# Kernel tuning notes

Measured on AMD Instinct MI355X. Metric: run time of the kernel, lower is better.

Reference implementation:

```python
import jax, jax.numpy as jnp
import numpy as np
import math

B, C, H, W = 16, 256, 96, 96
S = 3  # num_stages
OUT_C = 64


def _pos_encoding(c, h, w):
    # Faithful vectorization of generate_fixed_cosine_positional_encoding.
    pos_y = jnp.linspace(0.0, 1.0, h)
    pos_x = jnp.linspace(0.0, 1.0, w)
    py, px = jnp.meshgrid(pos_y, pos_x, indexing='ij')  # [H, W]
    i_vals = np.arange(0, c // 2, 2)                    # loop indices i
    freqs = jnp.exp(jnp.asarray(i_vals, jnp.float32) * -(math.log(10000.0) / (c // 2)))  # div_term[i//2]
    sin_part = jnp.sin(px[None] * freqs[:, None, None]) + jnp.sin(py[None] * freqs[:, None, None])
    cos_part = jnp.cos(px[None] * freqs[:, None, None]) + jnp.cos(py[None] * freqs[:, None, None])
    pe = jnp.zeros((c, h, w), jnp.float32)
    pe = pe.at[2 * i_vals].set(sin_part).at[2 * i_vals + 1].set(cos_part)
    return pe


def _nearest_resize(wmap, h, w):
    # torch F.interpolate(mode='nearest'): src_idx = floor(dst_idx * in/out)
    hw, ww = wmap.shape[-2], wmap.shape[-1]
    ih = (jnp.arange(h) * hw) // h
    iw = (jnp.arange(w) * ww) // w
    return wmap[..., ih[:, None], iw[None, :]]


def _conv1x1(x, w, b):
    return jnp.einsum('oc,bchw->bohw', w, x) + b[None, :, None, None]


def setup_inputs():
    key = jax.random.key(0)
    ks = jax.random.split(key, 12)
    sc = 0.3 / math.sqrt(C)
    return {
        'x1': jax.random.normal(ks[0], (B, C, H, W), jnp.float32),
        'x2': jax.random.normal(ks[1], (B, C, H, W), jnp.float32),
        'weight_vis': jax.random.uniform(ks[2], (B, H, W), jnp.float32),
        'weight_ir': jax.random.uniform(ks[3], (B, H, W), jnp.float32),
        'q_w': jax.random.normal(ks[4], (S, C, C), jnp.float32) * sc,
        'q_b': jnp.zeros((S, C), jnp.float32),
        'k_w': jax.random.normal(ks[5], (S, C, C), jnp.float32) * sc,
        'k_b': jnp.zeros((S, C), jnp.float32),
        'v_w': jax.random.normal(ks[6], (S, C, C), jnp.float32) * sc,
        'v_b': jnp.zeros((S, C), jnp.float32),
        'proj_w': jax.random.normal(ks[7], (OUT_C, C), jnp.float32) * sc,
        'proj_b': jnp.zeros((OUT_C,), jnp.float32),
    }


def reference(x1, x2, weight_vis, weight_ir, q_w, q_b, k_w, k_b, v_w, v_b, proj_w, proj_b):
    pe = _pos_encoding(x1.shape[1], x1.shape[2], x1.shape[3])  # combined_pos_encoding = pe1
    h, w = x1.shape[2], x1.shape[3]
    w_vis = _nearest_resize(weight_vis[:, None], h, w)  # [B,1,H,W]
    w_ir = _nearest_resize(weight_ir[:, None], h, w)
    fused = x1
    for i in range(S):
        x1 = x1 * w_vis
        x2 = x2 * w_ir
        q = _conv1x1(x1, q_w[i], q_b[i]) + pe[None]          # [B,C,H,W]
        k = _conv1x1(x2, k_w[i], k_b[i]) + pe[None]
        v = _conv1x1(x2, v_w[i], v_b[i])
        logits = jnp.einsum('bchw,bcgw->bchg', q, k)         # per-channel QK^T: [B,C,H,H]
        attn = jax.nn.softmax(logits, axis=-1)
        fused = jnp.einsum('bchg,bcgw->bchw', attn, v)       # [B,C,H,W]
        x1, x2 = fused, fused
    return _conv1x1(fused, proj_w, proj_b)                    # [B,64,H,W]
```

## Files before the change

### kernel.cpp

```cpp
#include <hip/hip_runtime.h>
#include <hip/hip_bf16.h>
#include <math.h>

#define NPOS 9216
#define PERB 2359296ull

typedef unsigned short u16;
typedef __attribute__((ext_vector_type(8))) short short8;
typedef __attribute__((ext_vector_type(4))) float f32x4;

__device__ inline u16 bfhi(float x) {
    unsigned int b = __float_as_uint(x);
    return (u16)((b + 0x7FFFu + ((b >> 16) & 1u)) >> 16);
}
__device__ inline float bf2f(u16 u) { return __uint_as_float(((unsigned int)u) << 16); }

typedef const __attribute__((address_space(1))) void* gvp;
typedef __attribute__((address_space(3))) void* lvp;
__device__ __forceinline__ void glds16(const void* g, void* l) {
    __builtin_amdgcn_global_load_lds((gvp)g, (lvp)l, 16, 0, 0);
}

__global__ __launch_bounds__(256) void tt_kernel(float* __restrict__ T)
{
    int idx = blockIdx.x * 256 + threadIdx.x;
    int c = idx / 96, p = idx - (idx / 96) * 96;
    int j = c >> 2, r = c & 3;
    float f = expf(-(float)(2 * j) * 0.07195578415f);
    float x = (float)p * (1.0f / 95.0f) * f;
    T[idx] = (r == 0) ? sinf(x) : (r == 1) ? cosf(x) : 0.0f;
}

__global__ __launch_bounds__(256) void wsplit(
    const float* __restrict__ qw, const float* __restrict__ kw,
    const float* __restrict__ vw, u16* __restrict__ whi, u16* __restrict__ wlo)
{
    int bid = blockIdx.x;
    int s = bid / 48, rem = bid % 48;
    int mat = rem / 16, rem2 = rem % 16;
    int mb = rem2 / 8, kb = rem2 % 8;
    const float* W = ((mat == 0) ? qw : (mat == 1) ? kw : vw) + (size_t)s * 65536;
    int t = threadIdx.x;
    int m = t >> 1, kh = (t & 1) * 16;
    const float* src = W + (size_t)(mb * 128 + m) * 256 + kb * 32 + kh;
    int s0 = kh >> 3;
    int sw = (m >> 1) & 3;
    size_t ob = (size_t)s * 196608 + (size_t)((mat * 2 + mb) * 8 + kb) * 4096
              + (size_t)m * 32;
    u16 hv[16], lv[16];
#pragma unroll
    for (int j = 0; j < 16; ++j) {
        float x = src[j];
        u16 h = bfhi(x);
        hv[j] = h;
        lv[j] = bfhi(x - bf2f(h));
    }
    *(uint4*)(whi + ob + ((s0 ^ sw) * 8))       = *(uint4*)hv;
    *(uint4*)(whi + ob + (((s0 + 1) ^ sw) * 8)) = *(uint4*)(hv + 8);
    *(uint4*)(wlo + ob + ((s0 ^ sw) * 8))       = *(uint4*)lv;
    *(uint4*)(wlo + ob + (((s0 + 1) ^ sw) * 8)) = *(uint4*)(lv + 8);
}

__global__ __launch_bounds__(512, 4) void gemm_qkv_mfma(
    const u16* __restrict__ whi, const u16* __restrict__ wlo,
    const float* __restrict__ srcq, const float* __restrict__ srckv,
    const float* __restrict__ qb, const float* __restrict__ kbias,
    const float* __restrict__ vb, const float* __restrict__ wvis,
    const float* __restrict__ wir, const float* __restrict__ Ttab,
    float* __restrict__ qo, float* __restrict__ ko, float* __restrict__ vo)
{
    __shared__ char LDSBUF[49152];
    u16* AH = (u16*)LDSBUF;
    u16* AL = AH + 8192;
    u16* BH = AL + 8192;
    u16* BL = BH + 4096;

    int t = threadIdx.x;
    int d = blockIdx.x + 3 * blockIdx.y;
    int role = (d & 7) * 27 + (d >> 3);
    int mat = role / 72, bn = role % 72;
    int b = blockIdx.z;

    const float* gB = ((mat == 0) ? srcq : srckv) + (size_t)b * PERB + bn * 128;
    const u16* gA0 = whi + (size_t)(mat * 2) * 32768;
    const u16* gA1 = wlo + (size_t)(mat * 2) * 32768;

    int wv = t >> 6;
    int wm = wv >> 1, wn = wv & 1;
    int rr = t & 15, gq = (t >> 4) & 3;

    int sxor = (gq ^ ((rr >> 1) & 3)) * 8;
    int offA0 = (wm * 64 + rr) * 32 + sxor;
    int offB0 = (wn * 64 + rr) * 32 + sxor;

    int arow = t >> 2, acol = (t & 3) * 8;
    size_t asrc0 = (size_t)arow * 32 + acol;
    size_t asrc1 = 32768 + (size_t)arow * 32 + acol;

    int bn_ = t & 127, bkh = t >> 7;
    int key = (bn_ >> 1) & 3;
    int wrB = bn_ * 32 + ((bkh ^ key) * 8);
    const float* bp = gB + (size_t)(bkh * 8) * NPOS + bn_;

    f32x4 acc[4][4];
#pragma unroll
    for (int i = 0; i < 4; ++i)
#pragma unroll
        for (int j = 0; j < 4; ++j) acc[i][j] = (f32x4){0.f, 0.f, 0.f, 0.f};

    float xv[8];
#pragma unroll
    for (int j = 0; j < 8; ++j) xv[j] = bp[(size_t)j * NPOS];

    for (int kq = 0; kq < 8; ++kq) {
        {
            glds16(gA0 + kq * 4096 + asrc0, &AH[t * 8]);
            glds16(gA0 + kq * 4096 + asrc1, &AH[t * 8 + 4096]);
            glds16(gA1 + kq * 4096 + asrc0, &AL[t * 8]);
            glds16(gA1 + kq * 4096 + asrc1, &AL[t * 8 + 4096]);
        }
        {
            u16 hv[8], lv[8];
#pragma unroll
            for (int j = 0; j < 8; ++j) {
                float x = xv[j];
                u16 h = bfhi(x);
                hv[j] = h;
                lv[j] = bfhi(x - bf2f(h));
            }
            *(uint4*)(&BH[wrB]) = *(uint4*)hv;
            *(uint4*)(&BL[wrB]) = *(uint4*)lv;
        }
        __syncthreads();

        if (kq < 7) {
#pragma unroll
            for (int j = 0; j < 8; ++j)
                xv[j] = bp[(size_t)((kq + 1) * 32 + j) * NPOS];
        }

        short8 bh[4], bl[4];
#pragma unroll
        for (int r = 0; r < 4; ++r) {
            bh[r] = *(const short8*)(&BH[offB0 + r * 512]);
            bl[r] = *(const short8*)(&BL[offB0 + r * 512]);
        }
#pragma unroll
        for (int f = 0; f < 4; ++f) {
            short8 ah = *(const short8*)(&AH[offA0 + f * 512]);
            short8 al = *(const short8*)(&AL[offA0 + f * 512]);
#pragma unroll
            for (int r = 0; r < 4; ++r) {
                acc[f][r] = __builtin_amdgcn_mfma_f32_16x16x32_bf16(ah, bh[r], acc[f][r], 0, 0, 0);
                acc[f][r] = __builtin_amdgcn_mfma_f32_16x16x32_bf16(ah, bl[r], acc[f][r], 0, 0, 0);
                acc[f][r] = __builtin_amdgcn_mfma_f32_16x16x32_bf16(al, bh[r], acc[f][r], 0, 0, 0);
            }
        }
        asm volatile("s_waitcnt lgkmcnt(0)" ::: "memory");
        __builtin_amdgcn_s_barrier();
        __builtin_amdgcn_sched_barrier(0);
    }

    float* SB = (float*)LDSBUF + (size_t)wv * (16 * 68);
    const float* wmap = ((mat == 0) ? wvis : wir) + (size_t)b * NPOS;
    const float* bias = (mat == 0) ? qb : (mat == 1) ? kbias : vb;
    float* outp = ((mat == 0) ? qo : (mat == 1) ? ko : vo) + (size_t)b * PERB;
    bool addpe = (mat != 2);

    int lane = t & 63;
    int lrow = lane >> 2;
    int lq   = lane & 3;
    int base_n = bn * 128 + wn * 64;

#pragma unroll
    for (int f = 0; f < 4; ++f) {
#pragma unroll
        for (int r = 0; r < 4; ++r)
#pragma unroll
            for (int ri = 0; ri < 4; ++ri)
                SB[(gq * 4 + ri) * 68 + (r * 16 + rr)] = acc[f][r][ri];
        int o = wm * 64 + f * 16 + lrow;
        float bo = bias[o];
        const float* tro = Ttab + o * 96;
        float* orow = outp + (size_t)o * NPOS;
#pragma unroll
        for (int qd = 0; qd < 4; ++qd) {
            int c0 = lq * 16 + qd * 4;
            int n = base_n + c0;
            float4 v4 = *(float4*)&SB[lrow * 68 + c0];
            float4 s4 = *(const float4*)&wmap[n];
            float4 o4;
            if (addpe) {
                int hh = n / 96, ww = n - hh * 96;
                float4 pw4 = *(const float4*)&tro[ww];
                float ph = tro[hh];
                o4.x = v4.x * s4.x + bo + pw4.x + ph;
                o4.y = v4.y * s4.y + bo + pw4.y + ph;
                o4.z = v4.z * s4.z + bo + pw4.z + ph;
                o4.w = v4.w * s4.w + bo + pw4.w + ph;
            } else {
                o4.x = v4.x * s4.x + bo;
                o4.y = v4.y * s4.y + bo;
                o4.z = v4.z * s4.z + bo;
                o4.w = v4.w * s4.w + bo;
            }
            *(float4*)&orow[n] = o4;
        }
    }
}

__global__ __launch_bounds__(192, 2) void attn_mfma(
    const float* __restrict__ q, const float* __restrict__ k,
    const float* __restrict__ v, float* __restrict__ fused)
{
    __shared__ char LB[76800];
    u16* QH = (u16*)LB;
    u16* QL = (u16*)(LB + 19200);
    u16* KH = (u16*)(LB + 38400);
    u16* KL = (u16*)(LB + 57600);
    float* OB = (float*)LB;

    int t = threadIdx.x;
    int bc = blockIdx.x;
    size_t base = (size_t)bc * NPOS;
    int wq = t >> 6, rr = t & 15, gq = (t >> 4) & 3;
    int sxor = (gq ^ ((rr >> 1) & 3)) * 8;

#pragma unroll
    for (int i = 0; i < 12; ++i) {
        int idx = i * 192 + t;
        int row = idx / 24, c4 = (idx % 24) * 4;
        int tile = c4 >> 5, kin = c4 & 31;
        int a = tile * 3072 + row * 32 + (((kin >> 3) ^ ((row >> 1) & 3)) << 3) + (kin & 7);
        float4 qv = *(const float4*)(q + base + row * 96 + c4);
        float4 kv = *(const float4*)(k + base + row * 96 + c4);
        unsigned int qh01, qh23, ql01, ql23, kh01, kh23, kl01, kl23;
        {
            u16 h0 = bfhi(qv.x), h1 = bfhi(qv.y), h2 = bfhi(qv.z), h3 = bfhi(qv.w);
            u16 l0 = bfhi(qv.x - bf2f(h0)), l1 = bfhi(qv.y - bf2f(h1));
            u16 l2 = bfhi(qv.z - bf2f(h2)), l3 = bfhi(qv.w - bf2f(h3));
            qh01 = (unsigned)h0 | ((unsigned)h1 << 16); qh23 = (unsigned)h2 | ((unsigned)h3 << 16);
            ql01 = (unsigned)l0 | ((unsigned)l1 << 16); ql23 = (unsigned)l2 | ((unsigned)l3 << 16);
        }
        {
            u16 h0 = bfhi(kv.x), h1 = bfhi(kv.y), h2 = bfhi(kv.z), h3 = bfhi(kv.w);
            u16 l0 = bfhi(kv.x - bf2f(h0)), l1 = bfhi(kv.y - bf2f(h1));
            u16 l2 = bfhi(kv.z - bf2f(h2)), l3 = bfhi(kv.w - bf2f(h3));
            kh01 = (unsigned)h0 | ((unsigned)h1 << 16); kh23 = (unsigned)h2 | ((unsigned)h3 << 16);
            kl01 = (unsigned)l0 | ((unsigned)l1 << 16); kl23 = (unsigned)l2 | ((unsigned)l3 << 16);
        }
        *(uint2*)(QH + a) = (uint2){qh01, qh23};
        *(uint2*)(QL + a) = (uint2){ql01, ql23};
        *(uint2*)(KH + a) = (uint2){kh01, kh23};
        *(uint2*)(KL + a) = (uint2){kl01, kl23};
    }
    __syncthreads();

    f32x4 acc[2][6];
#pragma unroll
    for (int mt = 0; mt < 2; ++mt)
#pragma unroll
        for (int nt = 0; nt < 6; ++nt) acc[mt][nt] = (f32x4){0.f, 0.f, 0.f, 0.f};

#pragma unroll
    for (int ks = 0; ks < 3; ++ks) {
        short8 qh2[2], ql2[2], kh6[6], kl6[6];
#pragma unroll
        for (int mt = 0; mt < 2; ++mt) {
            int ra = ks * 3072 + (wq * 32 + mt * 16 + rr) * 32 + sxor;
            qh2[mt] = *(const short8*)(QH + ra);
            ql2[mt] = *(const short8*)(QL + ra);
        }
#pragma unroll
        for (int nt = 0; nt < 6; ++nt) {
            int rb = ks * 3072 + (nt * 16 + rr) * 32 + sxor;
            kh6[nt] = *(const short8*)(KH + rb);
            kl6[nt] = *(const short8*)(KL + rb);
        }
#pragma unroll
        for (int mt = 0; mt < 2; ++mt)
#pragma unroll
            for (int nt = 0; nt < 6; ++nt) {
                acc[mt][nt] = __builtin_amdgcn_mfma_f32_16x16x32_bf16(qh2[mt], kh6[nt], acc[mt][nt], 0, 0, 0);
                acc[mt][nt] = __builtin_amdgcn_mfma_f32_16x16x32_bf16(qh2[mt], kl6[nt], acc[mt][nt], 0, 0, 0);
                acc[mt][nt] = __builtin_amdgcn_mfma_f32_16x16x32_bf16(ql2[mt], kh6[nt], acc[mt][nt], 0, 0, 0);
                acc[mt][nt] = __builtin_amdgcn_mfma_f32_16x16x32_bf16(ql2[mt], kl6[nt], acc[mt][nt], 0, 0, 0);
            }
    }

#pragma unroll
    for (int mt = 0; mt < 2; ++mt)
#pragma unroll
        for (int ri = 0; ri < 4; ++ri) {
            float mx = acc[mt][0][ri];
#pragma unroll
            for (int nt = 1; nt < 6; ++nt) mx = fmaxf(mx, acc[mt][nt][ri]);
            for (int dd = 1; dd < 16; dd <<= 1) mx = fmaxf(mx, __shfl_xor(mx, dd));
            float s = 0.0f;
#pragma unroll
            for (int nt = 0; nt < 6; ++nt) {
                float e = __expf(acc[mt][nt][ri] - mx);
                acc[mt][nt][ri] = e;
                s += e;
            }
            for (int dd = 1; dd < 16; dd <<= 1) s += __shfl_xor(s, dd);
            float inv = 1.0f / s;
#pragma unroll
            for (int nt = 0; nt < 6; ++nt) acc[mt][nt][ri] *= inv;
        }

    __syncthreads();

#pragma unroll
    for (int mt = 0; mt < 2; ++mt)
#pragma unroll
        for (int ri = 0; ri < 4; ++ri) {
            int row = wq * 32 + mt * 16 + gq * 4 + ri;
            int keyr = (row >> 1) & 3;
#pragma unroll
            for (int nt = 0; nt < 6; ++nt) {
                float val = acc[mt][nt][ri];
                u16 h = bfhi(val);
                u16 l = bfhi(val - bf2f(h));
                int slot = ((nt & 1) << 1) | (rr >> 3);
                int a = (nt >> 1) * 3072 + row * 32 + ((slot ^ keyr) << 3) + (rr & 7);
                QH[a] = h;
                QL[a] = l;
            }
        }
#pragma unroll
    for (int i = 0; i < 12; ++i) {
        int idx = i * 192 + t;
        int grow = idx / 24, c4 = (idx % 24) * 4;
        float4 vv = *(const float4*)(v + base + grow * 96 + c4);
        int tile = grow >> 5, kin = grow & 31;
        int slot = kin >> 3, off = kin & 7;
#pragma unroll
        for (int e = 0; e < 4; ++e) {
            int w = c4 + e;
            float val = (e == 0) ? vv.x : (e == 1) ? vv.y : (e == 2) ? vv.z : vv.w;
            u16 h = bfhi(val);
            u16 l = bfhi(val - bf2f(h));
            int a = tile * 3072 + w * 32 + ((slot ^ ((w >> 1) & 3)) << 3) + off;
            KH[a] = h;
            KL[a] = l;
        }
    }
    __syncthreads();

#pragma unroll
    for (int mt = 0; mt < 2; ++mt)
#pragma unroll
        for (int nt = 0; nt < 6; ++nt) acc[mt][nt] = (f32x4){0.f, 0.f, 0.f, 0.f};

#pragma unroll
    for (int ks = 0; ks < 3; ++ks) {
        short8 ph2[2], pl2[2], vh6[6], vl6[6];
#pragma unroll
        for (int mt = 0; mt < 2; ++mt) {
            int ra = ks * 3072 + (wq * 32 + mt * 16 + rr) * 32 + sxor;
            ph2[mt] = *(const short8*)(QH + ra);
            pl2[mt] = *(const short8*)(QL + ra);
        }
#pragma unroll
        for (int nt = 0; nt < 6; ++nt) {
            int rb = ks * 3072 + (nt * 16 + rr) * 32 + sxor;
            vh6[nt] = *(const short8*)(KH + rb);
            vl6[nt] = *(const short8*)(KL + rb);
        }
#pragma unroll
        for (int mt = 0; mt < 2; ++mt)
#pragma unroll
            for (int nt = 0; nt < 6; ++nt) {
                acc[mt][nt] = __builtin_amdgcn_mfma_f32_16x16x32_bf16(ph2[mt], vh6[nt], acc[mt][nt], 0, 0, 0);
                acc[mt][nt] = __builtin_amdgcn_mfma_f32_16x16x32_bf16(ph2[mt], vl6[nt], acc[mt][nt], 0, 0, 0);
                acc[mt][nt] = __builtin_amdgcn_mfma_f32_16x16x32_bf16(pl2[mt], vh6[nt], acc[mt][nt], 0, 0, 0);
            }
    }
    __syncthreads();

#pragma unroll
    for (int mt = 0; mt < 2; ++mt)
#pragma unroll
        for (int nt = 0; nt < 6; ++nt)
#pragma unroll
            for (int ri = 0; ri < 4; ++ri) {
                int row = wq * 32 + mt * 16 + gq * 4 + ri;
                OB[row * 100 + nt * 16 + rr] = acc[mt][nt][ri];
            }
    __syncthreads();
#pragma unroll
    for (int i = 0; i < 12; ++i) {
        int idx = i * 192 + t;
        int row = idx / 24, c4 = (idx % 24) * 4;
        float4 o = *(const float4*)&OB[row * 100 + c4];
        *(float4*)(fused + base + row * 96 + c4) = o;
    }
}

__global__ __launch_bounds__(256) void proj_kernel(
    const float* __restrict__ fused, const float* __restrict__ pw,
    const float* __restrict__ pb, float* __restrict__ out)
{
    __shared__ float As[16 * 68];
    __shared__ float Bs[16 * 128];

    int t  = threadIdx.x;
    int n0 = blockIdx.x * 128;
    int b  = blockIdx.y;
    const float* B = fused + (size_t)b * PERB;
    int tx = t & 15, ty = t >> 4;

    float acc[4][8];
#pragma unroll
    for (int i = 0; i < 4; ++i)
#pragma unroll
        for (int j = 0; j < 8; ++j) acc[i][j] = 0.0f;

    for (int k0 = 0; k0 < 256; k0 += 16) {
        {
            int m = t >> 2, c4 = (t & 3) * 4;
            float4 av = *(const float4*)(pw + (size_t)m * 256 + k0 + c4);
            As[(c4 + 0) * 68 + m] = av.x;
            As[(c4 + 1) * 68 + m] = av.y;
            As[(c4 + 2) * 68 + m] = av.z;
            As[(c4 + 3) * 68 + m] = av.w;
        }
#pragma unroll
        for (int l = 0; l < 2; ++l) {
            int f = t + l * 256;
            int c = f >> 5, n4 = (f & 31) * 4;
            *(float4*)(Bs + c * 128 + n4) =
                *(const float4*)(B + (size_t)(k0 + c) * NPOS + n0 + n4);
        }
        __syncthreads();
#pragma unroll
        for (int kk = 0; kk < 16; ++kk) {
            float a[4], bb[8];
            *(float4*)(&a[0])  = *(const float4*)(As + kk * 68 + ty * 4);
            *(float4*)(&bb[0]) = *(const float4*)(Bs + kk * 128 + tx * 8);
            *(float4*)(&bb[4]) = *(const float4*)(Bs + kk * 128 + tx * 8 + 4);
#pragma unroll
            for (int i = 0; i < 4; ++i)
#pragma unroll
                for (int j = 0; j < 8; ++j)
                    acc[i][j] = fmaf(a[i], bb[j], acc[i][j]);
        }
        __syncthreads();
    }

    int n = n0 + tx * 8;
#pragma unroll
    for (int i = 0; i < 4; ++i) {
        int o = ty * 4 + i;
        float bias = pb[o];
        float vals[8];
#pragma unroll
        for (int j = 0; j < 8; ++j) vals[j] = acc[i][j] + bias;
        float* op = out + ((size_t)b * 64 + o) * NPOS + n;
        *(float4*)(op)     = *(float4*)(&vals[0]);
        *(float4*)(op + 4) = *(float4*)(&vals[4]);
    }
}

extern "C" void kernel_launch(void* const* d_in, const int* in_sizes, int n_in,
                              void* d_out, int out_size, void* d_ws, size_t ws_size,
                              hipStream_t stream)
{
    const float* x1   = (const float*)d_in[0];
    const float* x2   = (const float*)d_in[1];
    const float* wvis = (const float*)d_in[2];
    const float* wir  = (const float*)d_in[3];
    const float* qw   = (const float*)d_in[4];
    const float* qb   = (const float*)d_in[5];
    const float* kw   = (const float*)d_in[6];
    const float* kb   = (const float*)d_in[7];
    const float* vw   = (const float*)d_in[8];
    const float* vb   = (const float*)d_in[9];
    const float* pw   = (const float*)d_in[10];
    const float* pb   = (const float*)d_in[11];
    float* out = (float*)d_out;

    float* ws = (float*)d_ws;
    size_t F = ws_size / 4;
    size_t fixed = 350000;
    size_t avail = (F > fixed) ? (F - fixed) : 0;
    int G = (int)(avail / (4 * PERB));
    if (G < 1) G = 1;
    if (G > 8) G = 8;

    float* ttab  = ws;
    float* qbuf  = ws + 24576;
    float* kbuf  = qbuf + (size_t)G * PERB;
    float* vbuf  = kbuf + (size_t)G * PERB;
    float* fbuf  = vbuf + (size_t)G * PERB;
    u16*   whiP  = (u16*)(fbuf + (size_t)G * PERB);
    u16*   wloP  = whiP + 589824;

    tt_kernel<<<dim3(96), 256, 0, stream>>>(ttab);
    wsplit<<<dim3(144), 256, 0, stream>>>(qw, kw, vw, whiP, wloP);

    for (int b0 = 0; b0 < 16; b0 += G) {
        int g = (16 - b0 < G) ? (16 - b0) : G;
        for (int s = 0; s < 3; ++s) {
            const float* sq  = (s == 0) ? (x1 + (size_t)b0 * PERB) : fbuf;
            const float* skv = (s == 0) ? (x2 + (size_t)b0 * PERB) : fbuf;
            gemm_qkv_mfma<<<dim3(3, 72, g), 512, 0, stream>>>(
                whiP + (size_t)s * 196608, wloP + (size_t)s * 196608,
                sq, skv,
                qb + (size_t)s * 256, kb + (size_t)s * 256, vb + (size_t)s * 256,
                wvis + (size_t)b0 * NPOS, wir + (size_t)b0 * NPOS,
                ttab, qbuf, kbuf, vbuf);
            attn_mfma<<<dim3(256 * g), 192, 0, stream>>>(qbuf, kbuf, vbuf, fbuf);
        }
        proj_kernel<<<dim3(72, g), 256, 0, stream>>>(
            fbuf, pw, pb, out + (size_t)b0 * 64 * NPOS);
    }
}
```

Before: 1.575 ms.

## Double-buffer weight tiles in LDS to prefetch next K-slice during MFMA

The QKV GEMM now keeps two LDS buffers for the hi/lo bf16 weight tiles. While the current K-slice is being computed, the async global-to-LDS loads for the next slice are already issued, and explicit vmcnt waits replace the plain __syncthreads. This is meant to hide weight-load latency behind MFMA work. The cost is that LDS per block grows from 48KB to 80KB, which may cut how many blocks fit on a CU and lower occupancy.

Result: slower. 2.080 ms (+32.0%).

```diff
diff --git a/kernel.cpp b/kernel.cpp
--- a/kernel.cpp
+++ b/kernel.cpp
@@ -69,10 +69,8 @@
     const float* __restrict__ wir, const float* __restrict__ Ttab,
     float* __restrict__ qo, float* __restrict__ ko, float* __restrict__ vo)
 {
-    __shared__ char LDSBUF[49152];
-    u16* AH = (u16*)LDSBUF;
-    u16* AL = AH + 8192;
-    u16* BH = AL + 8192;
+    __shared__ char LDSBUF[81920];
+    u16* BH = (u16*)(LDSBUF + 65536);
     u16* BL = BH + 4096;
 
     int t = threadIdx.x;
@@ -93,9 +91,8 @@
     int offA0 = (wm * 64 + rr) * 32 + sxor;
     int offB0 = (wn * 64 + rr) * 32 + sxor;
 
-    int arow = t >> 2, acol = (t & 3) * 8;
-    size_t asrc0 = (size_t)arow * 32 + acol;
-    size_t asrc1 = 32768 + (size_t)arow * 32 + acol;
+    size_t asrc0 = (size_t)t * 8;
+    size_t asrc1 = 32768 + (size_t)t * 8;
 
     int bn_ = t & 127, bkh = t >> 7;
     int key = (bn_ >> 1) & 3;
@@ -108,16 +105,27 @@
 #pragma unroll
         for (int j = 0; j < 4; ++j) acc[i][j] = (f32x4){0.f, 0.f, 0.f, 0.f};
 
+    {
+        u16* A = (u16*)LDSBUF;
+        glds16(gA0 + asrc0, &A[t * 8]);
+        glds16(gA0 + asrc1, &A[t * 8 + 4096]);
+        glds16(gA1 + asrc0, &A[t * 8 + 8192]);
+        glds16(gA1 + asrc1, &A[t * 8 + 12288]);
+    }
     float xv[8];
 #pragma unroll
     for (int j = 0; j < 8; ++j) xv[j] = bp[(size_t)j * NPOS];
 
+#pragma unroll
     for (int kq = 0; kq < 8; ++kq) {
-        {
-            glds16(gA0 + kq * 4096 + asrc0, &AH[t * 8]);
-            glds16(gA0 + kq * 4096 + asrc1, &AH[t * 8 + 4096]);
-            glds16(gA1 + kq * 4096 + asrc0, &AL[t * 8]);
-            glds16(gA1 + kq * 4096 + asrc1, &AL[t * 8 + 4096]);
+        const int cur = kq & 1, nxt = cur ^ 1;
+        u16* Acur = (u16*)(LDSBUF + cur * 32768);
+        if (kq < 7) {
+            u16* An = (u16*)(LDSBUF + nxt * 32768);
+            glds16(gA0 + (kq + 1) * 4096 + asrc0, &An[t * 8]);
+            glds16(gA0 + (kq + 1) * 4096 + asrc1, &An[t * 8 + 4096]);
+            glds16(gA1 + (kq + 1) * 4096 + asrc0, &An[t * 8 + 8192]);
+            glds16(gA1 + (kq + 1) * 4096 + asrc1, &An[t * 8 + 12288]);
         }
         {
             u16 hv[8], lv[8];
@@ -131,14 +139,17 @@
             *(uint4*)(&BH[wrB]) = *(uint4*)hv;
             *(uint4*)(&BL[wrB]) = *(uint4*)lv;
         }
-        __syncthreads();
-
+        if (kq < 7)
+            asm volatile("s_waitcnt vmcnt(4) lgkmcnt(0)" ::: "memory");
+        else
+            asm volatile("s_waitcnt vmcnt(0) lgkmcnt(0)" ::: "memory");
+        __builtin_amdgcn_s_barrier();
+        __builtin_amdgcn_sched_barrier(0);
         if (kq < 7) {
 #pragma unroll
             for (int j = 0; j < 8; ++j)
                 xv[j] = bp[(size_t)((kq + 1) * 32 + j) * NPOS];
         }
-
         short8 bh[4], bl[4];
 #pragma unroll
         for (int r = 0; r < 4; ++r) {
@@ -147,8 +158,8 @@
         }
 #pragma unroll
         for (int f = 0; f < 4; ++f) {
-            short8 ah = *(const short8*)(&AH[offA0 + f * 512]);
-            short8 al = *(const short8*)(&AL[offA0 + f * 512]);
+            short8 ah = *(const short8*)(&Acur[offA0 + f * 512]);
+            short8 al = *(const short8*)(&Acur[8192 + offA0 + f * 512]);
 #pragma unroll
             for (int r = 0; r < 4; ++r) {
                 acc[f][r] = __builtin_amdgcn_mfma_f32_16x16x32_bf16(ah, bh[r], acc[f][r], 0, 0, 0);
@@ -156,9 +167,7 @@
                 acc[f][r] = __builtin_amdgcn_mfma_f32_16x16x32_bf16(al, bh[r], acc[f][r], 0, 0, 0);
             }
         }
-        asm volatile("s_waitcnt lgkmcnt(0)" ::: "memory");
         __builtin_amdgcn_s_barrier();
-        __builtin_amdgcn_sched_barrier(0);
     }
 
     float* SB = (float*)LDSBUF + (size_t)wv * (16 * 68);
```
